# Optimization experiments

Hardware: AMD Instinct MI355X
Metric: run time of the kernel (lower is better)

## Reference

```python
import jax, jax.numpy as jnp
import numpy as np
import math

NUM_HEADS = 16
HEAD_DIM = 64
ROPE_BASE = 10000.0

def _rope_tables(T, dtype):
    # inv_freq: (D/2,), emb = cat([freqs, freqs]) -> (T, D)
    inv_freq = 1.0 / (ROPE_BASE ** (jnp.arange(0, HEAD_DIM, 2, dtype=jnp.float32) / HEAD_DIM))
    t = jnp.arange(T, dtype=jnp.float32)
    freqs = jnp.einsum('i,j->ij', t, inv_freq)          # (T, D/2)
    emb = jnp.concatenate([freqs, freqs], axis=-1)      # (T, D)
    return jnp.cos(emb).astype(dtype), jnp.sin(emb).astype(dtype)

def _rotate_half(x):
    # interleaved pair rotation: (x0,x1,x2,x3,...) -> (-x1,x0,-x3,x2,...)
    x1 = x[..., ::2]
    x2 = x[..., 1::2]
    return jnp.stack((-x2, x1), axis=-1).reshape(x.shape)

def setup_inputs() -> dict:
    key = jax.random.key(0)
    ks = jax.random.split(key, 9)
    B, T, C = 2, 2048, 1024
    s = 1.0 / math.sqrt(C)
    return {
        'x':  jax.random.normal(ks[0], (B, T, C), dtype=jnp.float32),
        'wq': jax.random.normal(ks[1], (C, C), dtype=jnp.float32) * s,
        'bq': jax.random.normal(ks[2], (C,), dtype=jnp.float32) * s,
        'wk': jax.random.normal(ks[3], (C, C), dtype=jnp.float32) * s,
        'bk': jax.random.normal(ks[4], (C,), dtype=jnp.float32) * s,
        'wv': jax.random.normal(ks[5], (C, C), dtype=jnp.float32) * s,
        'bv': jax.random.normal(ks[6], (C,), dtype=jnp.float32) * s,
        'wo': jax.random.normal(ks[7], (C, C), dtype=jnp.float32) * s,
        'bo': jax.random.normal(ks[8], (C,), dtype=jnp.float32) * s,
    }

def reference(x, wq, bq, wk, bk, wv, bv, wo, bo):
    B, T, C = x.shape
    H, D = NUM_HEADS, HEAD_DIM

    def heads(t):  # (B,T,C) -> (B,H,T,D)
        return t.reshape(B, T, H, D).transpose(0, 2, 1, 3)

    q = heads(x @ wq.T + bq)
    k = heads(x @ wk.T + bk)
    v = heads(x @ wv.T + bv)

    cos, sin = _rope_tables(T, x.dtype)                 # (T, D)
    cos = cos[None, None]                               # (1,1,T,D)
    sin = sin[None, None]
    q = q * cos + _rotate_half(q) * sin
    k = k * cos + _rotate_half(k) * sin

    scores = jnp.einsum('bhqd,bhkd->bhqk', q, k) / math.sqrt(D)
    attn = jax.nn.softmax(scores, axis=-1)
    out = jnp.einsum('bhqk,bhkd->bhqd', attn, v)        # (B,H,T,D)
    out = out.transpose(0, 2, 1, 3).reshape(B, T, C)
    return out @ wo.T + bo
```

## Files before the change

kernel.cpp:

```cpp
#include <hip/hip_runtime.h>
#include <cmath>

#define TSEQ 2048
#define CDIM 1024
#define NHEAD 16
#define HDIM 64

typedef _Float16 half8 __attribute__((ext_vector_type(8)));
typedef _Float16 half4 __attribute__((ext_vector_type(4)));
typedef _Float16 half2v __attribute__((ext_vector_type(2)));
typedef __fp16 fp16x2 __attribute__((ext_vector_type(2)));
typedef float f32x4 __attribute__((ext_vector_type(4)));

#define QSCALE   0.18033688011112042f
#define SHIFT_L2 12.984255368000671f

__device__ __forceinline__ void gload16(const void* g, void* l) {
    __builtin_amdgcn_global_load_lds((const __attribute__((address_space(1))) void*)g,
                                     (__attribute__((address_space(3))) void*)l, 16, 0, 0);
}

__device__ __forceinline__ half2v cvt_pk_f16(float a, float b) {
    fp16x2 r = __builtin_amdgcn_cvt_pkrtz(a, b);
    return __builtin_bit_cast(half2v, r);
}

__global__ __launch_bounds__(256) void cvt_kernel(
    const float* __restrict__ x, const float* __restrict__ wq, const float* __restrict__ wk,
    const float* __restrict__ wv, const float* __restrict__ wo, _Float16* __restrict__ dst)
{
    const int y = blockIdx.y;
    const float* src;
    size_t cnt, doff;
    if (y == 0) { src = x; cnt = 4194304; doff = 0; }
    else {
        cnt = 1048576; doff = 4194304 + (size_t)(y - 1) * 1048576;
        src = (y == 1) ? wq : (y == 2) ? wk : (y == 3) ? wv : wo;
    }
    size_t i = ((size_t)blockIdx.x * 256 + threadIdx.x) * 4;
    if (i >= cnt) return;
    const float4 v = *(const float4*)(src + i);
    half4 h;
    h[0] = (_Float16)v.x; h[1] = (_Float16)v.y; h[2] = (_Float16)v.z; h[3] = (_Float16)v.w;
    *(half4*)(dst + doff + i) = h;
}

__global__ __launch_bounds__(256) void qkv_mfma_kernel(
    const _Float16* __restrict__ xh,
    const _Float16* __restrict__ wqh, const _Float16* __restrict__ wkh, const _Float16* __restrict__ wvh,
    const float* __restrict__ bq, const float* __restrict__ bk, const float* __restrict__ bv,
    _Float16* __restrict__ Qh, _Float16* __restrict__ Kh, _Float16* __restrict__ Vth)
{
    __shared__ __align__(16) _Float16 As[64 * 32];
    __shared__ __align__(16) _Float16 Bs[128 * 32];
    const int tid = threadIdx.x;
    const int lane = tid & 63, wid = tid >> 6;
    const int z = blockIdx.z;
    const _Float16* wh = (z == 0) ? wqh : (z == 1) ? wkh : wvh;
    const int m0 = blockIdx.y << 6, n0 = blockIdx.x << 7;

    const int srow = tid >> 2;
    const int sch = (tid & 3) ^ ((srow >> 1) & 3);
    const _Float16* gA = xh + (size_t)(m0 + srow) * CDIM + sch * 8;
    const _Float16* gB = wh + (size_t)(n0 + srow) * CDIM + sch * 8;
    _Float16* lA = As + tid * 8;
    _Float16* lB = Bs + tid * 8;

    const int cq = lane & 15, kg = lane >> 4;
    const int rchunk = (kg ^ ((lane >> 1) & 3)) * 8;
    const _Float16* pA = As + cq * 32 + rchunk;
    const _Float16* pB = Bs + (wid * 32 + cq) * 32 + rchunk;

    f32x4 acc[4][2] = {};

    for (int k0 = 0; k0 < CDIM; k0 += 32) {
        __syncthreads();
        gload16(gA + k0, lA);
        gload16(gB + k0, lB);
        gload16(gB + (size_t)64 * CDIM + k0, lB + 2048);
        __syncthreads();
        half8 af[4], bf[2];
#pragma unroll
        for (int f = 0; f < 4; ++f) af[f] = *(const half8*)(pA + f * 512);
#pragma unroll
        for (int f = 0; f < 2; ++f) bf[f] = *(const half8*)(pB + f * 512);
#pragma unroll
        for (int i = 0; i < 4; ++i)
#pragma unroll
            for (int j = 0; j < 2; ++j)
                acc[i][j] = __builtin_amdgcn_mfma_f32_16x16x32_f16(af[i], bf[j], acc[i][j], 0, 0, 0);
    }

    if (z < 2) {
        const float* bias = z ? bk : bq;
        _Float16* dst = z ? Kh : Qh;
        const float qs = z ? 1.f : QSCALE;
#pragma unroll
        for (int fn = 0; fn < 2; ++fn) {
            int n = n0 + wid * 32 + fn * 16 + cq;
            int d = n & 63, h = n >> 6;
            float bs = bias[n];
            float fr = exp2f((float)(d & 31) * -0.41524101186092029f);
            float sgn = (d & 1) ? 1.f : -1.f;
#pragma unroll
            for (int fm = 0; fm < 4; ++fm) {
#pragma unroll
                for (int r = 0; r < 4; ++r) {
                    int m = m0 + fm * 16 + (kg << 2) + r;
                    int t = m & (TSEQ - 1), b = m >> 11;
                    float v = acc[fm][fn][r] + bs;
                    float prt = __shfl_xor(v, 1);
                    float sn, cs;
                    __sincosf((float)t * fr, &sn, &cs);
                    dst[(((size_t)(b * NHEAD + h)) * TSEQ + t) * HDIM + d] =
                        (_Float16)((v * cs + sgn * prt * sn) * qs);
                }
            }
        }
    } else {
#pragma unroll
        for (int fn = 0; fn < 2; ++fn) {
            int n = n0 + wid * 32 + fn * 16 + cq;
            int d = n & 63, h = n >> 6;
            float bs = bv[n];
#pragma unroll
            for (int fm = 0; fm < 4; ++fm) {
                int m = m0 + fm * 16 + (kg << 2);
                int t = m & (TSEQ - 1), b = m >> 11;
                half4 ov;
#pragma unroll
                for (int r = 0; r < 4; ++r) ov[r] = (_Float16)(acc[fm][fn][r] + bs);
                *(half4*)&Vth[(((size_t)(b * NHEAD + h)) * HDIM + d) * TSEQ + t] = ov;
            }
        }
    }
}

__global__ __launch_bounds__(256) void attn_mfma_kernel(
    const _Float16* __restrict__ Qh, const _Float16* __restrict__ Kh,
    const _Float16* __restrict__ Vth, _Float16* __restrict__ Ah)
{
    __shared__ __align__(16) _Float16 Ks[2 * 64 * 64];
    __shared__ __align__(16) _Float16 Vts[2 * 64 * 64];
    __shared__ __align__(16) _Float16 Ps[4 * 16 * 64];

    const int tid = threadIdx.x, lane = tid & 63, wid = tid >> 6;
    const int bh = blockIdx.y, q0 = blockIdx.x << 6;
    const size_t hb = (size_t)bh * TSEQ * HDIM;

    const int cq = lane & 15, kg = lane >> 4, lx = lane & 7;

    const _Float16* gq = Qh + hb + (size_t)(q0 + wid * 16 + cq) * HDIM + kg * 8;
    half8 aQ0 = *(const half8*)(gq);
    half8 aQ1 = *(const half8*)(gq + 32);

    const int srow = tid >> 3;
    const int sch = ((tid & 7) ^ (srow & 7)) * 8;
    const _Float16* gK = Kh + hb + (size_t)srow * HDIM + sch;
    const _Float16* gV = Vth + hb + (size_t)srow * TSEQ + sch;
    _Float16* lK = Ks + tid * 8;
    _Float16* lV = Vts + tid * 8;

    const int ch0 = (kg ^ lx) * 8, ch1 = ((4 + kg) ^ lx) * 8;
    _Float16* Pw = Ps + wid * 1024;
    const _Float16* prd = Pw + cq * 64;
    const int chp0 = (kg ^ lx) << 3;
    const int chp1 = ((4 + kg) ^ lx) << 3;

    half8 ones;
#pragma unroll
    for (int j = 0; j < 8; ++j) ones[j] = (_Float16)1.f;

    f32x4 o[4] = {};
    f32x4 o5 = {};
    const f32x4 shift_init = {-SHIFT_L2, -SHIFT_L2, -SHIFT_L2, -SHIFT_L2};

    gload16(gK, lK);
    gload16(gK + 32 * HDIM, lK + 2048);
    gload16(gV, lV);
    gload16(gV + 32 * TSEQ, lV + 2048);
    __syncthreads();

    for (int kt = 0; kt < TSEQ / 64; ++kt) {
        const int buf = kt & 1;
        if (kt + 1 < TSEQ / 64) {
            const int nb = (buf ^ 1) * 4096;
            gload16(gK + (size_t)(kt + 1) * 64 * HDIM, lK + nb);
            gload16(gK + (size_t)(kt + 1) * 64 * HDIM + 32 * HDIM, lK + nb + 2048);
            gload16(gV + (kt + 1) * 64, lV + nb);
            gload16(gV + (kt + 1) * 64 + 32 * TSEQ, lV + nb + 2048);
        }
        const _Float16* Kb = Ks + buf * 4096;
        const _Float16* Vb = Vts + buf * 4096;

        f32x4 sf[4];
        __builtin_amdgcn_s_setprio(1);
#pragma unroll
        for (int g = 0; g < 4; ++g) {
            const _Float16* krow = Kb + (g * 16 + cq) * 64;
            f32x4 zv = shift_init;
            zv = __builtin_amdgcn_mfma_f32_16x16x32_f16(*(const half8*)(krow + ch0), aQ0, zv, 0, 0, 0);
            zv = __builtin_amdgcn_mfma_f32_16x16x32_f16(*(const half8*)(krow + ch1), aQ1, zv, 0, 0, 0);
            sf[g] = zv;
        }
        __builtin_amdgcn_s_setprio(0);

        half4 ph[4];
#pragma unroll
        for (int g = 0; g < 4; ++g) {
            float p0 = __builtin_amdgcn_exp2f(sf[g][0]);
            float p1 = __builtin_amdgcn_exp2f(sf[g][1]);
            float p2 = __builtin_amdgcn_exp2f(sf[g][2]);
            float p3 = __builtin_amdgcn_exp2f(sf[g][3]);
            half2v lo = cvt_pk_f16(p0, p1);
            half2v hi = cvt_pk_f16(p2, p3);
            ph[g][0] = lo[0]; ph[g][1] = lo[1];
            ph[g][2] = hi[0]; ph[g][3] = hi[1];
        }

#pragma unroll
        for (int g = 0; g < 4; ++g)
            *(half4*)(Pw + cq * 64 + ((((g << 1) + (kg >> 1)) ^ lx) << 3) + ((kg & 1) << 2)) = ph[g];
        __threadfence_block();
        half8 ap0 = *(const half8*)(prd + chp0);
        half8 ap1 = *(const half8*)(prd + chp1);

        __builtin_amdgcn_s_setprio(1);
#pragma unroll
        for (int dg = 0; dg < 4; ++dg) {
            const _Float16* vrow = Vb + (dg * 16 + cq) * 64;
            o[dg] = __builtin_amdgcn_mfma_f32_16x16x32_f16(*(const half8*)(vrow + ch0), ap0, o[dg], 0, 0, 0);
            o[dg] = __builtin_amdgcn_mfma_f32_16x16x32_f16(*(const half8*)(vrow + ch1), ap1, o[dg], 0, 0, 0);
        }
        o5 = __builtin_amdgcn_mfma_f32_16x16x32_f16(ones, ap0, o5, 0, 0, 0);
        o5 = __builtin_amdgcn_mfma_f32_16x16x32_f16(ones, ap1, o5, 0, 0, 0);
        __builtin_amdgcn_s_setprio(0);
        __syncthreads();
    }

    const int b = bh >> 4, hh = bh & 15;
    const float inv = 1.f / o5[0];
    const int t = q0 + wid * 16 + cq;
    const size_t rowoff = ((size_t)b * TSEQ + t) * CDIM + hh * 64;
#pragma unroll
    for (int dg = 0; dg < 4; ++dg) {
        half4 ov;
#pragma unroll
        for (int r = 0; r < 4; ++r) ov[r] = (_Float16)(o[dg][r] * inv);
        *(half4*)&Ah[rowoff + dg * 16 + (kg << 2)] = ov;
    }
}

__global__ __launch_bounds__(256) void oproj_mfma_kernel(
    const _Float16* __restrict__ Ahh, const _Float16* __restrict__ woh,
    const float* __restrict__ bo, float* __restrict__ out)
{
    __shared__ __align__(16) _Float16 As[64 * 32];
    __shared__ __align__(16) _Float16 Bs[128 * 32];
    const int tid = threadIdx.x;
    const int lane = tid & 63, wid = tid >> 6;
    const int m0 = blockIdx.y << 6, n0 = blockIdx.x << 7;

    const int srow = tid >> 2;
    const int sch = (tid & 3) ^ ((srow >> 1) & 3);
    const _Float16* gA = Ahh + (size_t)(m0 + srow) * CDIM + sch * 8;
    const _Float16* gB = woh + (size_t)(n0 + srow) * CDIM + sch * 8;
    _Float16* lA = As + tid * 8;
    _Float16* lB = Bs + tid * 8;

    const int cq = lane & 15, kg = lane >> 4;
    const int rchunk = (kg ^ ((lane >> 1) & 3)) * 8;
    const _Float16* pA = As + cq * 32 + rchunk;
    const _Float16* pB = Bs + (wid * 32 + cq) * 32 + rchunk;

    f32x4 acc[4][2] = {};

    for (int k0 = 0; k0 < CDIM; k0 += 32) {
        __syncthreads();
        gload16(gA + k0, lA);
        gload16(gB + k0, lB);
        gload16(gB + (size_t)64 * CDIM + k0, lB + 2048);
        __syncthreads();
        half8 af[4], bf[2];
#pragma unroll
        for (int f = 0; f < 4; ++f) af[f] = *(const half8*)(pA + f * 512);
#pragma unroll
        for (int f = 0; f < 2; ++f) bf[f] = *(const half8*)(pB + f * 512);
#pragma unroll
        for (int i = 0; i < 4; ++i)
#pragma unroll
            for (int j = 0; j < 2; ++j)
                acc[i][j] = __builtin_amdgcn_mfma_f32_16x16x32_f16(af[i], bf[j], acc[i][j], 0, 0, 0);
    }

#pragma unroll
    for (int fn = 0; fn < 2; ++fn) {
        int n = n0 + wid * 32 + fn * 16 + cq;
        float bs = bo[n];
#pragma unroll
        for (int fm = 0; fm < 4; ++fm) {
#pragma unroll
            for (int r = 0; r < 4; ++r) {
                int m = m0 + fm * 16 + (kg << 2) + r;
                out[(size_t)m * CDIM + n] = acc[fm][fn][r] + bs;
            }
        }
    }
}

extern "C" void kernel_launch(void* const* d_in, const int* in_sizes, int n_in,
                              void* d_out, int out_size, void* d_ws, size_t ws_size,
                              hipStream_t stream) {
    (void)in_sizes; (void)n_in; (void)out_size; (void)ws_size;
    const float* x  = (const float*)d_in[0];
    const float* wq = (const float*)d_in[1];
    const float* bq = (const float*)d_in[2];
    const float* wk = (const float*)d_in[3];
    const float* bk = (const float*)d_in[4];
    const float* wv = (const float*)d_in[5];
    const float* bv = (const float*)d_in[6];
    const float* wo = (const float*)d_in[7];
    const float* bo = (const float*)d_in[8];
    float* out = (float*)d_out;

    _Float16* xh  = (_Float16*)d_ws;
    _Float16* wqh = xh + 4194304;
    _Float16* wkh = wqh + 1048576;
    _Float16* wvh = wkh + 1048576;
    _Float16* woh = wvh + 1048576;
    _Float16* Qh  = woh + 1048576;
    _Float16* Kh  = Qh + 4194304;
    _Float16* Vth = Kh + 4194304;
    _Float16* Ah  = Vth + 4194304;

    cvt_kernel<<<dim3(4096, 5), 256, 0, stream>>>(x, wq, wk, wv, wo, xh);
    qkv_mfma_kernel<<<dim3(8, 64, 3), 256, 0, stream>>>(xh, wqh, wkh, wvh, bq, bk, bv, Qh, Kh, Vth);
    attn_mfma_kernel<<<dim3(32, 32), 256, 0, stream>>>(Qh, Kh, Vth, Ah);
    oproj_mfma_kernel<<<dim3(8, 64), 256, 0, stream>>>(Ah, woh, bo, out);
}
```

Baseline: 138.9 us.

## Double-buffer GEMM K-tiles and move attention to 32x32 MFMA with register P

```diff
diff --git a/kernel.cpp b/kernel.cpp
--- a/kernel.cpp
+++ b/kernel.cpp
@@ -8,9 +8,10 @@
 
 typedef _Float16 half8 __attribute__((ext_vector_type(8)));
 typedef _Float16 half4 __attribute__((ext_vector_type(4)));
-typedef _Float16 half2v __attribute__((ext_vector_type(2)));
 typedef __fp16 fp16x2 __attribute__((ext_vector_type(2)));
 typedef float f32x4 __attribute__((ext_vector_type(4)));
+typedef float f32x16 __attribute__((ext_vector_type(16)));
+typedef unsigned int u32x4 __attribute__((ext_vector_type(4)));
 
 #define QSCALE   0.18033688011112042f
 #define SHIFT_L2 12.984255368000671f
@@ -20,9 +21,9 @@
                                      (__attribute__((address_space(3))) void*)l, 16, 0, 0);
 }
 
-__device__ __forceinline__ half2v cvt_pk_f16(float a, float b) {
+__device__ __forceinline__ unsigned int cvtpk_u32(float a, float b) {
     fp16x2 r = __builtin_amdgcn_cvt_pkrtz(a, b);
-    return __builtin_bit_cast(half2v, r);
+    return __builtin_bit_cast(unsigned int, r);
 }
 
 __global__ __launch_bounds__(256) void cvt_kernel(
@@ -51,44 +52,68 @@
     const float* __restrict__ bq, const float* __restrict__ bk, const float* __restrict__ bv,
     _Float16* __restrict__ Qh, _Float16* __restrict__ Kh, _Float16* __restrict__ Vth)
 {
-    __shared__ __align__(16) _Float16 As[64 * 32];
-    __shared__ __align__(16) _Float16 Bs[128 * 32];
+    __shared__ __align__(16) _Float16 As[2 * 64 * 64];
+    __shared__ __align__(16) _Float16 Bs[2 * 128 * 64];
     const int tid = threadIdx.x;
     const int lane = tid & 63, wid = tid >> 6;
     const int z = blockIdx.z;
     const _Float16* wh = (z == 0) ? wqh : (z == 1) ? wkh : wvh;
     const int m0 = blockIdx.y << 6, n0 = blockIdx.x << 7;
 
-    const int srow = tid >> 2;
-    const int sch = (tid & 3) ^ ((srow >> 1) & 3);
-    const _Float16* gA = xh + (size_t)(m0 + srow) * CDIM + sch * 8;
-    const _Float16* gB = wh + (size_t)(n0 + srow) * CDIM + sch * 8;
+    const int srow = tid >> 3;
+    const int sch = ((tid & 7) ^ (srow & 7)) * 8;
+    const _Float16* gA = xh + (size_t)(m0 + srow) * CDIM + sch;
+    const _Float16* gB = wh + (size_t)(n0 + srow) * CDIM + sch;
     _Float16* lA = As + tid * 8;
     _Float16* lB = Bs + tid * 8;
 
     const int cq = lane & 15, kg = lane >> 4;
-    const int rchunk = (kg ^ ((lane >> 1) & 3)) * 8;
-    const _Float16* pA = As + cq * 32 + rchunk;
-    const _Float16* pB = Bs + (wid * 32 + cq) * 32 + rchunk;
+    const int cx = cq & 7;
 
     f32x4 acc[4][2] = {};
 
-    for (int k0 = 0; k0 < CDIM; k0 += 32) {
+    gload16(gA, lA);                 gload16(gA + (size_t)32 * CDIM, lA + 2048);
+    gload16(gB, lB);                 gload16(gB + (size_t)32 * CDIM, lB + 2048);
+    gload16(gB + (size_t)64 * CDIM, lB + 4096);
+    gload16(gB + (size_t)96 * CDIM, lB + 6144);
+    __syncthreads();
+
+    for (int k0 = 0; k0 < CDIM; k0 += 64) {
+        const int buf = (k0 >> 6) & 1;
+        if (k0 + 64 < CDIM) {
+            const int na = (buf ^ 1) * 4096, nb = (buf ^ 1) * 8192;
+            gload16(gA + k0 + 64, lA + na);
+            gload16(gA + (size_t)32 * CDIM + k0 + 64, lA + na + 2048);
+            gload16(gB + k0 + 64, lB + nb);
+            gload16(gB + (size_t)32 * CDIM + k0 + 64, lB + nb + 2048);
+            gload16(gB + (size_t)64 * CDIM + k0 + 64, lB + nb + 4096);
+            gload16(gB + (size_t)96 * CDIM + k0 + 64, lB + nb + 6144);
+        }
+        const _Float16* Ab = As + buf * 4096;
+        const _Float16* Bb = Bs + buf * 8192;
+
+        half8 af[4][2], bf[2][2];
+#pragma unroll
+        for (int i = 0; i < 4; ++i)
+#pragma unroll
+            for (int ks = 0; ks < 2; ++ks)
+                af[i][ks] = *(const half8*)(Ab + (i * 16 + cq) * 64 + (((4 * ks + kg)) ^ cx) * 8);
+#pragma unroll
+        for (int j = 0; j < 2; ++j)
+#pragma unroll
+            for (int ks = 0; ks < 2; ++ks)
+                bf[j][ks] = *(const half8*)(Bb + (wid * 32 + j * 16 + cq) * 64 + (((4 * ks + kg)) ^ cx) * 8);
+
+        __builtin_amdgcn_s_setprio(1);
+#pragma unroll
+        for (int ks = 0; ks < 2; ++ks)
+#pragma unroll
+            for (int i = 0; i < 4; ++i)
+#pragma unroll
+                for (int j = 0; j < 2; ++j)
+                    acc[i][j] = __builtin_amdgcn_mfma_f32_16x16x32_f16(af[i][ks], bf[j][ks], acc[i][j], 0, 0, 0);
+        __builtin_amdgcn_s_setprio(0);
         __syncthreads();
-        gload16(gA + k0, lA);
-        gload16(gB + k0, lB);
-        gload16(gB + (size_t)64 * CDIM + k0, lB + 2048);
-        __syncthreads();
-        half8 af[4], bf[2];
-#pragma unroll
-        for (int f = 0; f < 4; ++f) af[f] = *(const half8*)(pA + f * 512);
-#pragma unroll
-        for (int f = 0; f < 2; ++f) bf[f] = *(const half8*)(pB + f * 512);
-#pragma unroll
-        for (int i = 0; i < 4; ++i)
-#pragma unroll
-            for (int j = 0; j < 2; ++j)
-                acc[i][j] = __builtin_amdgcn_mfma_f32_16x16x32_f16(af[i], bf[j], acc[i][j], 0, 0, 0);
     }
 
     if (z < 2) {
@@ -142,17 +167,20 @@
 {
     __shared__ __align__(16) _Float16 Ks[2 * 64 * 64];
     __shared__ __align__(16) _Float16 Vts[2 * 64 * 64];
-    __shared__ __align__(16) _Float16 Ps[4 * 16 * 64];
 
     const int tid = threadIdx.x, lane = tid & 63, wid = tid >> 6;
-    const int bh = blockIdx.y, q0 = blockIdx.x << 6;
+    const int bh = blockIdx.y, q0 = blockIdx.x << 7;
     const size_t hb = (size_t)bh * TSEQ * HDIM;
 
-    const int cq = lane & 15, kg = lane >> 4, lx = lane & 7;
-
-    const _Float16* gq = Qh + hb + (size_t)(q0 + wid * 16 + cq) * HDIM + kg * 8;
-    half8 aQ0 = *(const half8*)(gq);
-    half8 aQ1 = *(const half8*)(gq + 32);
+    const int ql = lane & 31;
+    const int hi = lane >> 5;
+    const int lx = lane & 7;
+
+    const int qrow = q0 + wid * 32 + ql;
+    const _Float16* gq = Qh + hb + (size_t)qrow * HDIM + hi * 8;
+    half8 bQ[4];
+#pragma unroll
+    for (int ks = 0; ks < 4; ++ks) bQ[ks] = *(const half8*)(gq + ks * 16);
 
     const int srow = tid >> 3;
     const int sch = ((tid & 7) ^ (srow & 7)) * 8;
@@ -161,19 +189,11 @@
     _Float16* lK = Ks + tid * 8;
     _Float16* lV = Vts + tid * 8;
 
-    const int ch0 = (kg ^ lx) * 8, ch1 = ((4 + kg) ^ lx) * 8;
-    _Float16* Pw = Ps + wid * 1024;
-    const _Float16* prd = Pw + cq * 64;
-    const int chp0 = (kg ^ lx) << 3;
-    const int chp1 = ((4 + kg) ^ lx) << 3;
-
-    half8 ones;
-#pragma unroll
-    for (int j = 0; j < 8; ++j) ones[j] = (_Float16)1.f;
-
-    f32x4 o[4] = {};
-    f32x4 o5 = {};
-    const f32x4 shift_init = {-SHIFT_L2, -SHIFT_L2, -SHIFT_L2, -SHIFT_L2};
+    f32x16 o0 = {}, o1 = {};
+    float l_run = 0.f;
+    f32x16 sinit;
+#pragma unroll
+    for (int i = 0; i < 16; ++i) sinit[i] = -SHIFT_L2;
 
     gload16(gK, lK);
     gload16(gK + 32 * HDIM, lK + 2048);
@@ -193,61 +213,71 @@
         const _Float16* Kb = Ks + buf * 4096;
         const _Float16* Vb = Vts + buf * 4096;
 
-        f32x4 sf[4];
+        f32x16 s0 = sinit, s1 = sinit;
         __builtin_amdgcn_s_setprio(1);
 #pragma unroll
-        for (int g = 0; g < 4; ++g) {
-            const _Float16* krow = Kb + (g * 16 + cq) * 64;
-            f32x4 zv = shift_init;
-            zv = __builtin_amdgcn_mfma_f32_16x16x32_f16(*(const half8*)(krow + ch0), aQ0, zv, 0, 0, 0);
-            zv = __builtin_amdgcn_mfma_f32_16x16x32_f16(*(const half8*)(krow + ch1), aQ1, zv, 0, 0, 0);
-            sf[g] = zv;
+        for (int ks = 0; ks < 4; ++ks) {
+            half8 k0 = *(const half8*)(Kb + ql * 64 + ((2 * ks + hi) ^ lx) * 8);
+            half8 k1 = *(const half8*)(Kb + (32 + ql) * 64 + ((2 * ks + hi) ^ lx) * 8);
+            s0 = __builtin_amdgcn_mfma_f32_32x32x16_f16(k0, bQ[ks], s0, 0, 0, 0);
+            s1 = __builtin_amdgcn_mfma_f32_32x32x16_f16(k1, bQ[ks], s1, 0, 0, 0);
         }
         __builtin_amdgcn_s_setprio(0);
 
-        half4 ph[4];
-#pragma unroll
-        for (int g = 0; g < 4; ++g) {
-            float p0 = __builtin_amdgcn_exp2f(sf[g][0]);
-            float p1 = __builtin_amdgcn_exp2f(sf[g][1]);
-            float p2 = __builtin_amdgcn_exp2f(sf[g][2]);
-            float p3 = __builtin_amdgcn_exp2f(sf[g][3]);
-            half2v lo = cvt_pk_f16(p0, p1);
-            half2v hi = cvt_pk_f16(p2, p3);
-            ph[g][0] = lo[0]; ph[g][1] = lo[1];
-            ph[g][2] = hi[0]; ph[g][3] = hi[1];
-        }
-
-#pragma unroll
-        for (int g = 0; g < 4; ++g)
-            *(half4*)(Pw + cq * 64 + ((((g << 1) + (kg >> 1)) ^ lx) << 3) + ((kg & 1) << 2)) = ph[g];
-        __threadfence_block();
-        half8 ap0 = *(const half8*)(prd + chp0);
-        half8 ap1 = *(const half8*)(prd + chp1);
+        f32x16 p0, p1;
+#pragma unroll
+        for (int i = 0; i < 16; ++i) p0[i] = __builtin_amdgcn_exp2f(s0[i]);
+#pragma unroll
+        for (int i = 0; i < 16; ++i) p1[i] = __builtin_amdgcn_exp2f(s1[i]);
+        float ls = 0.f;
+#pragma unroll
+        for (int i = 0; i < 16; ++i) ls += p0[i] + p1[i];
+        l_run += ls;
+
+        half8 bP[4];
+#pragma unroll
+        for (int g = 0; g < 2; ++g) {
+            const f32x16& p = g ? p1 : p0;
+            unsigned int a0 = cvtpk_u32(p[0], p[1]),   a1 = cvtpk_u32(p[2], p[3]);
+            unsigned int b0 = cvtpk_u32(p[4], p[5]),   b1 = cvtpk_u32(p[6], p[7]);
+            unsigned int c0 = cvtpk_u32(p[8], p[9]),   c1 = cvtpk_u32(p[10], p[11]);
+            unsigned int d0 = cvtpk_u32(p[12], p[13]), d1 = cvtpk_u32(p[14], p[15]);
+            unsigned int sA = hi ? a0 : b0, sB = hi ? a1 : b1;
+            unsigned int rA = __shfl_xor(sA, 32), rB = __shfl_xor(sB, 32);
+            u32x4 w0 = { hi ? rA : a0, hi ? rB : a1, hi ? b0 : rA, hi ? b1 : rB };
+            unsigned int sC = hi ? c0 : d0, sD = hi ? c1 : d1;
+            unsigned int rC = __shfl_xor(sC, 32), rD = __shfl_xor(sD, 32);
+            u32x4 w1 = { hi ? rC : c0, hi ? rD : c1, hi ? d0 : rC, hi ? d1 : rD };
+            bP[2 * g]     = __builtin_bit_cast(half8, w0);
+            bP[2 * g + 1] = __builtin_bit_cast(half8, w1);
+        }
 
         __builtin_amdgcn_s_setprio(1);
 #pragma unroll
-        for (int dg = 0; dg < 4; ++dg) {
-            const _Float16* vrow = Vb + (dg * 16 + cq) * 64;
-            o[dg] = __builtin_amdgcn_mfma_f32_16x16x32_f16(*(const half8*)(vrow + ch0), ap0, o[dg], 0, 0, 0);
-            o[dg] = __builtin_amdgcn_mfma_f32_16x16x32_f16(*(const half8*)(vrow + ch1), ap1, o[dg], 0, 0, 0);
-        }
-        o5 = __builtin_amdgcn_mfma_f32_16x16x32_f16(ones, ap0, o5, 0, 0, 0);
-        o5 = __builtin_amdgcn_mfma_f32_16x16x32_f16(ones, ap1, o5, 0, 0, 0);
+        for (int ks = 0; ks < 4; ++ks) {
+            half8 v0 = *(const half8*)(Vb + ql * 64 + ((2 * ks + hi) ^ lx) * 8);
+            half8 v1 = *(const half8*)(Vb + (32 + ql) * 64 + ((2 * ks + hi) ^ lx) * 8);
+            o0 = __builtin_amdgcn_mfma_f32_32x32x16_f16(v0, bP[ks], o0, 0, 0, 0);
+            o1 = __builtin_amdgcn_mfma_f32_32x32x16_f16(v1, bP[ks], o1, 0, 0, 0);
+        }
         __builtin_amdgcn_s_setprio(0);
         __syncthreads();
     }
 
     const int b = bh >> 4, hh = bh & 15;
-    const float inv = 1.f / o5[0];
-    const int t = q0 + wid * 16 + cq;
-    const size_t rowoff = ((size_t)b * TSEQ + t) * CDIM + hh * 64;
-#pragma unroll
-    for (int dg = 0; dg < 4; ++dg) {
-        half4 ov;
-#pragma unroll
-        for (int r = 0; r < 4; ++r) ov[r] = (_Float16)(o[dg][r] * inv);
-        *(half4*)&Ah[rowoff + dg * 16 + (kg << 2)] = ov;
+    const float l_tot = l_run + __shfl_xor(l_run, 32);
+    const float inv = 1.f / l_tot;
+    const size_t rowoff = ((size_t)b * TSEQ + qrow) * CDIM + hh * 64;
+#pragma unroll
+    for (int dg = 0; dg < 2; ++dg) {
+        const f32x16& o = dg ? o1 : o0;
+#pragma unroll
+        for (int j = 0; j < 4; ++j) {
+            half4 ov;
+#pragma unroll
+            for (int c = 0; c < 4; ++c) ov[c] = (_Float16)(o[4 * j + c] * inv);
+            *(half4*)&Ah[rowoff + dg * 32 + j * 8 + hi * 4] = ov;
+        }
     }
 }
 
@@ -255,42 +285,66 @@
     const _Float16* __restrict__ Ahh, const _Float16* __restrict__ woh,
     const float* __restrict__ bo, float* __restrict__ out)
 {
-    __shared__ __align__(16) _Float16 As[64 * 32];
-    __shared__ __align__(16) _Float16 Bs[128 * 32];
+    __shared__ __align__(16) _Float16 As[2 * 64 * 64];
+    __shared__ __align__(16) _Float16 Bs[2 * 128 * 64];
     const int tid = threadIdx.x;
     const int lane = tid & 63, wid = tid >> 6;
     const int m0 = blockIdx.y << 6, n0 = blockIdx.x << 7;
 
-    const int srow = tid >> 2;
-    const int sch = (tid & 3) ^ ((srow >> 1) & 3);
-    const _Float16* gA = Ahh + (size_t)(m0 + srow) * CDIM + sch * 8;
-    const _Float16* gB = woh + (size_t)(n0 + srow) * CDIM + sch * 8;
+    const int srow = tid >> 3;
+    const int sch = ((tid & 7) ^ (srow & 7)) * 8;
+    const _Float16* gA = Ahh + (size_t)(m0 + srow) * CDIM + sch;
+    const _Float16* gB = woh + (size_t)(n0 + srow) * CDIM + sch;
     _Float16* lA = As + tid * 8;
     _Float16* lB = Bs + tid * 8;
 
     const int cq = lane & 15, kg = lane >> 4;
-    const int rchunk = (kg ^ ((lane >> 1) & 3)) * 8;
-    const _Float16* pA = As + cq * 32 + rchunk;
-    const _Float16* pB = Bs + (wid * 32 + cq) * 32 + rchunk;
+    const int cx = cq & 7;
 
     f32x4 acc[4][2] = {};
 
-    for (int k0 = 0; k0 < CDIM; k0 += 32) {
+    gload16(gA, lA);                 gload16(gA + (size_t)32 * CDIM, lA + 2048);
+    gload16(gB, lB);                 gload16(gB + (size_t)32 * CDIM, lB + 2048);
+    gload16(gB + (size_t)64 * CDIM, lB + 4096);
+    gload16(gB + (size_t)96 * CDIM, lB + 6144);
+    __syncthreads();
+
+    for (int k0 = 0; k0 < CDIM; k0 += 64) {
+        const int buf = (k0 >> 6) & 1;
+        if (k0 + 64 < CDIM) {
+            const int na = (buf ^ 1) * 4096, nb = (buf ^ 1) * 8192;
+            gload16(gA + k0 + 64, lA + na);
+            gload16(gA + (size_t)32 * CDIM + k0 + 64, lA + na + 2048);
+            gload16(gB + k0 + 64, lB + nb);
+            gload16(gB + (size_t)32 * CDIM + k0 + 64, lB + nb + 2048);
+            gload16(gB + (size_t)64 * CDIM + k0 + 64, lB + nb + 4096);
+            gload16(gB + (size_t)96 * CDIM + k0 + 64, lB + nb + 6144);
+        }
+        const _Float16* Ab = As + buf * 4096;
+        const _Float16* Bb = Bs + buf * 8192;
+
+        half8 af[4][2], bf[2][2];
+#pragma unroll
+        for (int i = 0; i < 4; ++i)
+#pragma unroll
+            for (int ks = 0; ks < 2; ++ks)
+                af[i][ks] = *(const half8*)(Ab + (i * 16 + cq) * 64 + (((4 * ks + kg)) ^ cx) * 8);
+#pragma unroll
+        for (int j = 0; j < 2; ++j)
+#pragma unroll
+            for (int ks = 0; ks < 2; ++ks)
+                bf[j][ks] = *(const half8*)(Bb + (wid * 32 + j * 16 + cq) * 64 + (((4 * ks + kg)) ^ cx) * 8);
+
+        __builtin_amdgcn_s_setprio(1);
+#pragma unroll
+        for (int ks = 0; ks < 2; ++ks)
+#pragma unroll
+            for (int i = 0; i < 4; ++i)
+#pragma unroll
+                for (int j = 0; j < 2; ++j)
+                    acc[i][j] = __builtin_amdgcn_mfma_f32_16x16x32_f16(af[i][ks], bf[j][ks], acc[i][j], 0, 0, 0);
+        __builtin_amdgcn_s_setprio(0);
         __syncthreads();
-        gload16(gA + k0, lA);
-        gload16(gB + k0, lB);
-        gload16(gB + (size_t)64 * CDIM + k0, lB + 2048);
-        __syncthreads();
-        half8 af[4], bf[2];
-#pragma unroll
-        for (int f = 0; f < 4; ++f) af[f] = *(const half8*)(pA + f * 512);
-#pragma unroll
-        for (int f = 0; f < 2; ++f) bf[f] = *(const half8*)(pB + f * 512);
-#pragma unroll
-        for (int i = 0; i < 4; ++i)
-#pragma unroll
-            for (int j = 0; j < 2; ++j)
-                acc[i][j] = __builtin_amdgcn_mfma_f32_16x16x32_f16(af[i], bf[j], acc[i][j], 0, 0, 0);
     }
 
 #pragma unroll
@@ -335,6 +389,6 @@
 
     cvt_kernel<<<dim3(4096, 5), 256, 0, stream>>>(x, wq, wk, wv, wo, xh);
     qkv_mfma_kernel<<<dim3(8, 64, 3), 256, 0, stream>>>(xh, wqh, wkh, wvh, bq, bk, bv, Qh, Kh, Vth);
-    attn_mfma_kernel<<<dim3(32, 32), 256, 0, stream>>>(Qh, Kh, Vth, Ah);
+    attn_mfma_kernel<<<dim3(16, 32), 256, 0, stream>>>(Qh, Kh, Vth, Ah);
     oproj_mfma_kernel<<<dim3(8, 64), 256, 0, stream>>>(Ah, woh, bo, out);
 }
```

Result: faster. 128.1 us (-7.8%).
